# Performance work log

Measured on AMD Instinct MI355X. Metric: run time of the kernel, lower is better.

The kernel has to match this reference:

```python
import jax, jax.numpy as jnp
import numpy as np

DIM = 384
HEADS = 12
WH, WW = 7, 7
N = WH * WW
HEAD_DIM = DIM // HEADS
SCALE = HEAD_DIM ** -0.5


def _double_step_seq(step1, len1, step2, len2):
    seq1 = np.arange(0, step1 * len1, step1)
    seq2 = np.arange(0, step2 * len2, step2)
    return (seq1[:, None] + seq2[None, :]).reshape(1, -1)


def _rel_position_index():
    coords = _double_step_seq(2 * WW - 1, WH, 1, WW)  # (1, N)
    idx = coords + coords.T                            # (N, N)
    idx = idx[:, ::-1].copy()                          # flip along dim 1
    return jnp.asarray(idx, dtype=jnp.int32)

REL_IDX = _rel_position_index()


def setup_inputs() -> dict:
    key = jax.random.key(0)
    ks = jax.random.split(key, 6)
    B_ = 4096
    x = jax.random.normal(ks[0], (B_, N, DIM), dtype=jnp.float32)
    mask = jnp.zeros((64, N, N), dtype=jnp.float32)
    qkv_w = jax.random.normal(ks[1], (3 * DIM, DIM), dtype=jnp.float32) * 0.02
    qkv_b = jax.random.normal(ks[2], (3 * DIM,), dtype=jnp.float32) * 0.02
    proj_w = jax.random.normal(ks[3], (DIM, DIM), dtype=jnp.float32) * 0.02
    proj_b = jax.random.normal(ks[4], (DIM,), dtype=jnp.float32) * 0.02
    bias_table = jax.random.normal(ks[5], (169, HEADS), dtype=jnp.float32) * 0.02
    return {"x": x, "mask": mask, "qkv_w": qkv_w, "qkv_b": qkv_b,
            "proj_w": proj_w, "proj_b": proj_b, "bias_table": bias_table}


def reference(x, mask, qkv_w, qkv_b, proj_w, proj_b, bias_table):
    B_, n, C = x.shape
    # qkv projection: (B_, N, 3C) -> (3, B_, H, N, d)
    qkv = (x @ qkv_w.T + qkv_b).reshape(B_, n, 3, HEADS, HEAD_DIM)
    qkv = jnp.transpose(qkv, (2, 0, 3, 1, 4))
    q, k, v = qkv[0], qkv[1], qkv[2]
    q = q * SCALE
    attn = jnp.einsum('bhnd,bhmd->bhnm', q, k)  # (B_, H, N, N)
    # gathered relative position bias: (H, N, N)
    rel_bias = bias_table[REL_IDX.reshape(-1)].reshape(n, n, HEADS)
    rel_bias = jnp.transpose(rel_bias, (2, 0, 1))
    attn = attn + rel_bias[None]
    nW = mask.shape[0]
    attn = attn.reshape(B_ // nW, nW, HEADS, n, n) + mask[None, :, None]
    attn = attn.reshape(B_, HEADS, n, n)
    attn = jax.nn.softmax(attn, axis=-1)
    out = jnp.einsum('bhnm,bhmd->bnhd', attn, v).reshape(B_, n, C)
    out = out @ proj_w.T + proj_b
    return out
```

## Files before the change

### kernel.cpp

```cpp
#include <hip/hip_runtime.h>
#include <hip/hip_bf16.h>

#define NTOK 49
#define DIMC 384
#define NH 12
#define QSCALE 0.17677669529663687f

typedef __attribute__((ext_vector_type(8))) short short8;
typedef __attribute__((ext_vector_type(4))) float f32x4;
typedef unsigned int u32;

#define KS_OFF  0
#define VT_OFF  8192
#define PS_OFF  12288
#define QA_OFF  16384
#define BT_OFF  18432
#define QB_OFF  20464
#define SL_TOT  21616

#define NQFRAG (NH * 6 * 12)
#define WQB_SHORTS (NQFRAG * 512)
#define WPB_SHORTS (3 * 6 * 8192)
#define MB_TILES 1568
#define AV_BYTES ((size_t)MB_TILES * 6 * 16384)

__device__ __forceinline__ short f2bf(float f) {
    __bf16 h = (__bf16)f;
    return __builtin_bit_cast(short, h);
}
__device__ __forceinline__ float bf2f(short s) {
    u32 u = ((u32)(unsigned short)s) << 16;
    return __builtin_bit_cast(float, u);
}
__device__ __forceinline__ int cof(int p) { return 13 * (p / 7) + (p % 7); }

__device__ __forceinline__ void gld_lds16(const void* g, void* l) {
    __builtin_amdgcn_global_load_lds(
        (const __attribute__((address_space(1))) u32*)g,
        (__attribute__((address_space(3))) u32*)l, 16, 0, 0);
}

__device__ __forceinline__ short8 gather_bf(const float* __restrict__ w, int row, int k0) {
    const float* p = w + row * DIMC + k0;
    float4 a = *(const float4*)p;
    float4 b = *(const float4*)(p + 4);
    short8 r;
    r[0]=f2bf(a.x); r[1]=f2bf(a.y); r[2]=f2bf(a.z); r[3]=f2bf(a.w);
    r[4]=f2bf(b.x); r[5]=f2bf(b.y); r[6]=f2bf(b.z); r[7]=f2bf(b.w);
    return r;
}

__global__ void prep_weights(const float* __restrict__ qw, const float* __restrict__ pw,
                             short* __restrict__ wqb, short* __restrict__ wpb) {
    int gt = blockIdx.x * blockDim.x + threadIdx.x;
    if (gt < NQFRAG * 64) {
        int F = gt >> 6, lane = gt & 63;
        int h = F / 72, r = F % 72;
        int nt = r / 12, ks = r % 12;
        int l15 = lane & 15, l4 = lane >> 4;
        int grow = (nt >> 1) * DIMC + h * 32 + (nt & 1) * 16 + l15;
        const float* src = qw + grow * DIMC + ks * 32 + l4 * 8;
        short8 o;
        #pragma unroll
        for (int e = 0; e < 8; ++e) o[e] = f2bf(src[e]);
        *(short8*)(wqb + gt * 8) = o;
    } else if (gt < NQFRAG * 64 + 3 * 6 * 128 * 8) {
        int t2 = gt - NQFRAG * 64;
        int g  = t2 & 7;
        int r  = (t2 >> 3) & 127;
        int kc = (t2 >> 10) % 6;
        int nb = t2 / 6144;
        int k0 = kc * 64 + ((g ^ (r & 7)) << 3);
        const float* src = pw + (nb * 128 + r) * DIMC + k0;
        short8 o;
        #pragma unroll
        for (int e = 0; e < 8; ++e) o[e] = f2bf(src[e]);
        *(short8*)(wpb + (nb * 6 + kc) * 8192 + r * 64 + g * 8) = o;
    }
}

__global__ __launch_bounds__(256, 2)
void winattn_fused(const float* __restrict__ x, const float* __restrict__ mask,
                   const float* __restrict__ qkv_b, const float* __restrict__ bias_table,
                   const short* __restrict__ wqb, char* __restrict__ avb)
{
    __shared__ short SL[SL_TOT] __attribute__((aligned(128)));

    const int tid  = threadIdx.x;
    const int wv   = tid >> 6;
    const int lane = tid & 63;
    const int l15  = lane & 15;
    const int l4   = lane >> 4;
    const int win  = blockIdx.x;

    for (int i = tid; i < 169 * NH; i += 256) SL[BT_OFF + i] = f2bf(bias_table[i]);
    for (int i = tid; i < 3 * DIMC; i += 256) SL[QB_OFF + i] = f2bf(qkv_b[i]);

    short8 xf[12];
    {
        const int row = wv * 16 + l15;
        const bool valid = row < NTOK;
        const float* xr = x + (size_t)win * (NTOK * DIMC) + row * DIMC;
        #pragma unroll
        for (int ks = 0; ks < 12; ++ks) {
            short8 r;
            if (valid) {
                float4 a = *(const float4*)(xr + ks * 32 + l4 * 8);
                float4 b = *(const float4*)(xr + ks * 32 + l4 * 8 + 4);
                r[0]=f2bf(a.x); r[1]=f2bf(a.y); r[2]=f2bf(a.z); r[3]=f2bf(a.w);
                r[4]=f2bf(b.x); r[5]=f2bf(b.y); r[6]=f2bf(b.z); r[7]=f2bf(b.w);
            } else {
                r = (short8)0;
            }
            xf[ks] = r;
        }
    }

    u32 mvp[4][2];
    int bidx[4][4];
    {
        const float* maskp = mask + (size_t)(win & 63) * (NTOK * NTOK);
        #pragma unroll
        for (int t = 0; t < 4; ++t) {
            int m = t * 16 + l15;
            float pad = (m < NTOK) ? 0.f : -1e30f;
            #pragma unroll
            for (int rp = 0; rp < 2; ++rp) {
                float v[2];
                #pragma unroll
                for (int e = 0; e < 2; ++e) {
                    int i = wv * 16 + l4 * 4 + rp * 2 + e;
                    v[e] = ((i < NTOK && m < NTOK) ? maskp[i * NTOK + m] : 0.f) + pad;
                }
                mvp[t][rp] = (u32)(unsigned short)f2bf(v[0]) |
                             ((u32)(unsigned short)f2bf(v[1]) << 16);
            }
        }
        int cofi[4], cofm[4];
        #pragma unroll
        for (int t = 0; t < 4; ++t) {
            int m = t * 16 + l15;
            cofm[t] = cof(48 - (m < NTOK ? m : 48));
        }
        #pragma unroll
        for (int reg = 0; reg < 4; ++reg) {
            int i = wv * 16 + l4 * 4 + reg;
            cofi[reg] = cof(i < NTOK ? i : 48);
        }
        #pragma unroll
        for (int t = 0; t < 4; ++t)
            #pragma unroll
            for (int reg = 0; reg < 4; ++reg)
                bidx[t][reg] = (cofi[reg] + cofm[t]) * NH;
    }

    const f32x4 zf = (f32x4){0.f, 0.f, 0.f, 0.f};

    __syncthreads();

    auto qkv_head = [&](int h) {
        const int p = h & 1;
        f32x4 qa[6];
        #pragma unroll
        for (int nt = 0; nt < 6; ++nt) qa[nt] = zf;
        const short* wq_h = wqb + (size_t)h * 36864 + lane * 8;
        #pragma unroll
        for (int c = 0; c < 6; ++c) {
            short8 bfr[12];
            #pragma unroll
            for (int j = 0; j < 12; ++j)
                bfr[j] = *(const short8*)(wq_h + (((j >> 1) * 12) + 2 * c + (j & 1)) * 512);
            #pragma unroll
            for (int j = 0; j < 12; ++j)
                qa[j >> 1] = __builtin_amdgcn_mfma_f32_16x16x32_bf16(
                    xf[2 * c + (j & 1)], bfr[j], qa[j >> 1], 0, 0, 0);
        }
        #pragma unroll
        for (int nt = 0; nt < 6; ++nt) {
            const int sub = nt >> 1;
            const int colw = (nt & 1) * 16 + l15;
            const float bias = bf2f(SL[QB_OFF + sub * DIMC + h * 32 + colw]);
            #pragma unroll
            for (int reg = 0; reg < 4; ++reg) {
                const int rl = l4 * 4 + reg;
                const int tokg = wv * 16 + rl;
                float val = qa[nt][reg] + bias;
                if (sub == 0) {
                    int byt = rl * 64 + ((colw << 1) ^ ((rl & 3) << 4));
                    SL[QA_OFF + wv * 512 + (byt >> 1)] = f2bf(val * QSCALE);
                } else if (sub == 1) {
                    int byt = tokg * 128 + ((colw << 1) ^ ((tokg & 7) << 4));
                    SL[KS_OFF + p * 4096 + (byt >> 1)] = f2bf(val);
                } else {
                    int byt = colw * 128 + ((tokg << 1) ^ ((colw & 7) << 4));
                    SL[VT_OFF + p * 2048 + (byt >> 1)] = f2bf(val);
                }
            }
        }
        asm volatile("s_waitcnt lgkmcnt(0)" ::: "memory");
        __builtin_amdgcn_s_barrier();
        __builtin_amdgcn_sched_barrier(0);
    };

    auto attn_head = [&](int hh) {
        const int pp = hh & 1;
        short8 aq;
        {
            int byt = l15 * 64 + ((l4 * 16) ^ ((l15 & 3) << 4));
            aq = *(const short8*)&SL[QA_OFF + wv * 512 + (byt >> 1)];
        }
        f32x4 sc[4];
        #pragma unroll
        for (int t = 0; t < 4; ++t) {
            int row = t * 16 + l15;
            int byt = row * 128 + ((l4 * 16) ^ ((row & 7) << 4));
            short8 bk = *(const short8*)&SL[KS_OFF + pp * 4096 + (byt >> 1)];
            sc[t] = __builtin_amdgcn_mfma_f32_16x16x32_bf16(aq, bk, zf, 0, 0, 0);
        }
        float p[4][4];
        #pragma unroll
        for (int t = 0; t < 4; ++t) {
            #pragma unroll
            for (int reg = 0; reg < 4; ++reg) {
                u32 pk = mvp[t][reg >> 1];
                float mval = bf2f((short)((reg & 1) ? (pk >> 16) : (pk & 0xffff)));
                float bt = bf2f(SL[BT_OFF + bidx[t][reg] + hh]);
                p[t][reg] = sc[t][reg] + mval + bt;
            }
        }
        #pragma unroll
        for (int reg = 0; reg < 4; ++reg) {
            float mx = fmaxf(fmaxf(p[0][reg], p[1][reg]), fmaxf(p[2][reg], p[3][reg]));
            #pragma unroll
            for (int off = 8; off >= 1; off >>= 1) mx = fmaxf(mx, __shfl_xor(mx, off, 64));
            float s0 = 0.f;
            #pragma unroll
            for (int t = 0; t < 4; ++t) { p[t][reg] = __expf(p[t][reg] - mx); s0 += p[t][reg]; }
            #pragma unroll
            for (int off = 8; off >= 1; off >>= 1) s0 += __shfl_xor(s0, off, 64);
            float rs = 1.f / s0;
            #pragma unroll
            for (int t = 0; t < 4; ++t) p[t][reg] *= rs;
        }
        #pragma unroll
        for (int t = 0; t < 4; ++t)
            #pragma unroll
            for (int reg = 0; reg < 4; ++reg) {
                int r = l4 * 4 + reg;
                int byt = r * 128 + ((((t * 16 + l15) << 1)) ^ ((r & 7) << 4));
                SL[PS_OFF + wv * 1024 + (byt >> 1)] = f2bf(p[t][reg]);
            }
        f32x4 av[2];
        av[0] = zf; av[1] = zf;
        #pragma unroll
        for (int kst = 0; kst < 2; ++kst) {
            short8 pa;
            {
                int byt = l15 * 128 + (((kst * 64 + l4 * 16)) ^ ((l15 & 7) << 4));
                pa = *(const short8*)&SL[PS_OFF + wv * 1024 + (byt >> 1)];
            }
            #pragma unroll
            for (int dt = 0; dt < 2; ++dt) {
                int d = dt * 16 + l15;
                int byt = d * 128 + (((kst * 64 + l4 * 16)) ^ ((d & 7) << 4));
                short8 bv = *(const short8*)&SL[VT_OFF + pp * 2048 + (byt >> 1)];
                av[dt] = __builtin_amdgcn_mfma_f32_16x16x32_bf16(pa, bv, av[dt], 0, 0, 0);
            }
        }
        #pragma unroll
        for (int dt = 0; dt < 2; ++dt)
            #pragma unroll
            for (int reg = 0; reg < 4; ++reg) {
                int tok = wv * 16 + l4 * 4 + reg;
                if (tok < NTOK) {
                    int gt = win * NTOK + tok;
                    int mb = gt >> 7, r = gt & 127;
                    int inner = ((((hh & 1) << 6) | ((dt * 16 + l15) << 1))) ^ ((r & 7) << 4);
                    *(short*)(avb + (size_t)(mb * 6 + (hh >> 1)) * 16384 + r * 128 + inner)
                        = f2bf(av[dt][reg]);
                }
            }
    };

    qkv_head(0);
    #pragma unroll 1
    for (int h = 1; h < NH; ++h) {
        attn_head(h - 1);
        qkv_head(h);
    }
    attn_head(NH - 1);
}

__global__ __launch_bounds__(256, 2)
void proj_gemm(const char* __restrict__ avb, const short* __restrict__ wpb,
               const float* __restrict__ proj_b, float* __restrict__ out)
{
    __shared__ char LC[2][32768] __attribute__((aligned(128)));

    const int tid = threadIdx.x;
    const int wv = tid >> 6, lane = tid & 63;
    const int l15 = lane & 15, l4 = lane >> 4;
    const int wr = wv >> 1, wc = wv & 1;
    const int mb = blockIdx.x / 3, nb = blockIdx.x % 3;

    const char* asrc = avb + (size_t)mb * 6 * 16384;
    const char* bsrc = (const char*)wpb + (size_t)nb * 6 * 16384;

    f32x4 acc[4][4];
    #pragma unroll
    for (int mi = 0; mi < 4; ++mi)
        #pragma unroll
        for (int ni = 0; ni < 4; ++ni) acc[mi][ni] = (f32x4){0.f, 0.f, 0.f, 0.f};

    #pragma unroll
    for (int it = 0; it < 4; ++it) {
        int L = (wv * 4 + it) * 1024;
        gld_lds16(asrc + L + lane * 16, &LC[0][L]);
        gld_lds16(bsrc + L + lane * 16, &LC[0][16384 + L]);
    }

    #pragma unroll
    for (int kc = 0; kc < 6; ++kc) {
        __builtin_amdgcn_sched_barrier(0);
        asm volatile("s_waitcnt vmcnt(0)" ::: "memory");
        __builtin_amdgcn_s_barrier();
        __builtin_amdgcn_sched_barrier(0);
        if (kc < 5) {
            #pragma unroll
            for (int it = 0; it < 4; ++it) {
                int L = (wv * 4 + it) * 1024;
                gld_lds16(asrc + (kc + 1) * 16384 + L + lane * 16, &LC[(kc + 1) & 1][L]);
                gld_lds16(bsrc + (kc + 1) * 16384 + L + lane * 16, &LC[(kc + 1) & 1][16384 + L]);
            }
        }
        const char* bufp = LC[kc & 1];
        __builtin_amdgcn_s_setprio(1);
        #pragma unroll
        for (int ksub = 0; ksub < 2; ++ksub) {
            short8 a[4], b[4];
            #pragma unroll
            for (int mi = 0; mi < 4; ++mi) {
                int row = wr * 64 + mi * 16 + l15;
                a[mi] = *(const short8*)(bufp + row * 128 +
                        ((ksub * 64 + l4 * 16) ^ ((row & 7) << 4)));
            }
            #pragma unroll
            for (int ni = 0; ni < 4; ++ni) {
                int row = wc * 64 + ni * 16 + l15;
                b[ni] = *(const short8*)(bufp + 16384 + row * 128 +
                        ((ksub * 64 + l4 * 16) ^ ((row & 7) << 4)));
            }
            #pragma unroll
            for (int mi = 0; mi < 4; ++mi)
                #pragma unroll
                for (int ni = 0; ni < 4; ++ni)
                    acc[mi][ni] = __builtin_amdgcn_mfma_f32_16x16x32_bf16(
                        a[mi], b[ni], acc[mi][ni], 0, 0, 0);
        }
        __builtin_amdgcn_s_setprio(0);
    }

    float pb[4];
    #pragma unroll
    for (int ni = 0; ni < 4; ++ni) pb[ni] = proj_b[nb * 128 + wc * 64 + ni * 16 + l15];
    #pragma unroll
    for (int mi = 0; mi < 4; ++mi) {
        #pragma unroll
        for (int ni = 0; ni < 4; ++ni) {
            #pragma unroll
            for (int reg = 0; reg < 4; ++reg) {
                size_t row = (size_t)(mb * 128 + wr * 64 + mi * 16 + l4 * 4 + reg);
                out[row * DIMC + nb * 128 + wc * 64 + ni * 16 + l15] = acc[mi][ni][reg] + pb[ni];
            }
        }
    }
}

__global__ __launch_bounds__(256, 2)
void winattn_fallback(const float* __restrict__ x, const float* __restrict__ mask,
                      const float* __restrict__ qkv_w, const float* __restrict__ qkv_b,
                      const float* __restrict__ proj_w, const float* __restrict__ proj_b,
                      const float* __restrict__ bias_table, float* __restrict__ out)
{
    __shared__ short SL[26624] __attribute__((aligned(128)));
    const int tid = threadIdx.x, wv = tid >> 6, lane = tid & 63;
    const int l15 = lane & 15, l4 = lane >> 4;
    const int win = blockIdx.x;
    const int xbase = win * (NTOK * DIMC);
    const int KSo = 0, VTo = 2048, PSo = 4096, QAo = 8192;

    short8 xf[12];
    {
        const int row = wv * 16 + l15;
        const bool valid = row < NTOK;
        const float* xr = x + xbase + row * DIMC;
        #pragma unroll
        for (int ks = 0; ks < 12; ++ks)
            xf[ks] = valid ? gather_bf(xr, 0, ks * 32 + l4 * 8) : (short8)0;
    }
    float mv[4][4]; int bidx[4][4]; float negm[4];
    {
        const float* maskp = mask + (win & 63) * (NTOK * NTOK);
        int cofi[4], cofm[4];
        #pragma unroll
        for (int t = 0; t < 4; ++t) {
            int m = t * 16 + l15;
            negm[t] = (m < NTOK) ? 0.f : -1e30f;
            cofm[t] = cof(48 - (m < NTOK ? m : 48));
            #pragma unroll
            for (int reg = 0; reg < 4; ++reg) {
                int i = wv * 16 + l4 * 4 + reg;
                mv[t][reg] = (i < NTOK && m < NTOK) ? maskp[i * NTOK + m] : 0.f;
            }
        }
        #pragma unroll
        for (int reg = 0; reg < 4; ++reg) {
            int i = wv * 16 + l4 * 4 + reg;
            cofi[reg] = cof(i < NTOK ? i : 48);
        }
        #pragma unroll
        for (int t = 0; t < 4; ++t)
            #pragma unroll
            for (int reg = 0; reg < 4; ++reg) bidx[t][reg] = (cofi[reg] + cofm[t]) * NH;
    }
    f32x4 pacc[24];
    #pragma unroll
    for (int t = 0; t < 24; ++t) pacc[t] = (f32x4){0.f, 0.f, 0.f, 0.f};
    const f32x4 zf = (f32x4){0.f, 0.f, 0.f, 0.f};
    __syncthreads();

    #pragma unroll 1
    for (int h = 0; h < NH; ++h) {
        f32x4 qa[6];
        #pragma unroll
        for (int nt = 0; nt < 6; ++nt) qa[nt] = zf;
        #pragma unroll
        for (int nt = 0; nt < 6; ++nt) {
            const int grow = (nt >> 1) * DIMC + h * 32 + (nt & 1) * 16 + l15;
            #pragma unroll
            for (int ks = 0; ks < 12; ++ks) {
                short8 b = gather_bf(qkv_w, grow, ks * 32 + l4 * 8);
                qa[nt] = __builtin_amdgcn_mfma_f32_16x16x32_bf16(xf[ks], b, qa[nt], 0, 0, 0);
            }
        }
        #pragma unroll
        for (int nt = 0; nt < 6; ++nt) {
            const int sub = nt >> 1;
            const int colw = (nt & 1) * 16 + l15;
            const float bias = qkv_b[sub * DIMC + h * 32 + colw];
            #pragma unroll
            for (int reg = 0; reg < 4; ++reg) {
                const int tokg = wv * 16 + l4 * 4 + reg;
                float val = qa[nt][reg] + bias;
                if (sub == 0) {
                    int byt = tokg * 64 + ((colw << 1) ^ ((tokg & 3) << 4));
                    SL[QAo + (byt >> 1)] = f2bf(val * QSCALE);
                } else if (sub == 1) {
                    int byt = tokg * 64 + ((colw << 1) ^ ((tokg & 3) << 4));
                    SL[KSo + (byt >> 1)] = f2bf(val);
                } else {
                    int byt = colw * 128 + ((tokg << 1) ^ ((colw & 7) << 4));
                    SL[VTo + (byt >> 1)] = f2bf(val);
                }
            }
        }
        __syncthreads();
        short8 aq;
        { int row = wv*16+l15; int byt = row*64 + ((l4*16) ^ ((row&3)<<4));
          aq = *(const short8*)&SL[QAo + (byt>>1)]; }
        f32x4 sc[4];
        #pragma unroll
        for (int t = 0; t < 4; ++t) {
            int row = t*16+l15; int byt = row*64 + ((l4*16) ^ ((row&3)<<4));
            short8 bk = *(const short8*)&SL[KSo + (byt>>1)];
            sc[t] = __builtin_amdgcn_mfma_f32_16x16x32_bf16(aq, bk, zf, 0, 0, 0);
        }
        float p[4][4];
        #pragma unroll
        for (int t = 0; t < 4; ++t)
            #pragma unroll
            for (int reg = 0; reg < 4; ++reg)
                p[t][reg] = sc[t][reg] + mv[t][reg] + bias_table[bidx[t][reg] + h] + negm[t];
        #pragma unroll
        for (int reg = 0; reg < 4; ++reg) {
            float mx = fmaxf(fmaxf(p[0][reg], p[1][reg]), fmaxf(p[2][reg], p[3][reg]));
            #pragma unroll
            for (int off = 8; off >= 1; off >>= 1) mx = fmaxf(mx, __shfl_xor(mx, off, 64));
            float s0 = 0.f;
            #pragma unroll
            for (int t = 0; t < 4; ++t) { p[t][reg] = __expf(p[t][reg] - mx); s0 += p[t][reg]; }
            #pragma unroll
            for (int off = 8; off >= 1; off >>= 1) s0 += __shfl_xor(s0, off, 64);
            float rs = 1.f / s0;
            #pragma unroll
            for (int t = 0; t < 4; ++t) p[t][reg] *= rs;
        }
        #pragma unroll
        for (int t = 0; t < 4; ++t)
            #pragma unroll
            for (int reg = 0; reg < 4; ++reg) {
                int row = wv*16 + l4*4 + reg;
                int byt = row*128 + (((t*16+l15) << 1) ^ ((row&7)<<4));
                SL[PSo + (byt>>1)] = f2bf(p[t][reg]);
            }
        f32x4 av[2]; av[0] = zf; av[1] = zf;
        #pragma unroll
        for (int kst = 0; kst < 2; ++kst) {
            short8 pa;
            { int row = wv*16+l15; int byt = row*128 + ((kst*64+l4*16) ^ ((row&7)<<4));
              pa = *(const short8*)&SL[PSo + (byt>>1)]; }
            #pragma unroll
            for (int dt = 0; dt < 2; ++dt) {
                int d = dt*16+l15; int byt = d*128 + ((kst*64+l4*16) ^ ((d&7)<<4));
                short8 bv = *(const short8*)&SL[VTo + (byt>>1)];
                av[dt] = __builtin_amdgcn_mfma_f32_16x16x32_bf16(pa, bv, av[dt], 0, 0, 0);
            }
        }
        __syncthreads();
        #pragma unroll
        for (int dt = 0; dt < 2; ++dt)
            #pragma unroll
            for (int reg = 0; reg < 4; ++reg) {
                int row = wv*16 + l4*4 + reg;
                int byt = row*64 + (((dt*16+l15) << 1) ^ ((row&3)<<4));
                SL[QAo + (byt>>1)] = f2bf(av[dt][reg]);
            }
        __syncthreads();
        short8 aa;
        { int row = wv*16+l15; int byt = row*64 + ((l4*16) ^ ((row&3)<<4));
          aa = *(const short8*)&SL[QAo + (byt>>1)]; }
        #pragma unroll
        for (int nt = 0; nt < 24; ++nt) {
            short8 bp = gather_bf(proj_w, nt * 16 + l15, h * 32 + l4 * 8);
            pacc[nt] = __builtin_amdgcn_mfma_f32_16x16x32_bf16(aa, bp, pacc[nt], 0, 0, 0);
        }
    }
    {
        float* op = out + xbase;
        #pragma unroll
        for (int nt = 0; nt < 24; ++nt) {
            const float pb = proj_b[nt * 16 + l15];
            #pragma unroll
            for (int reg = 0; reg < 4; ++reg) {
                const int i = wv * 16 + l4 * 4 + reg;
                if (i < NTOK) op[i * DIMC + nt * 16 + l15] = pacc[nt][reg] + pb;
            }
        }
    }
}

extern "C" void kernel_launch(void* const* d_in, const int* in_sizes, int n_in,
                              void* d_out, int out_size, void* d_ws, size_t ws_size,
                              hipStream_t stream) {
    const float* x          = (const float*)d_in[0];
    const float* mask       = (const float*)d_in[1];
    const float* qkv_w      = (const float*)d_in[2];
    const float* qkv_b      = (const float*)d_in[3];
    const float* proj_w     = (const float*)d_in[4];
    const float* proj_b     = (const float*)d_in[5];
    const float* bias_table = (const float*)d_in[6];
    float* out = (float*)d_out;

    const size_t need = (size_t)WQB_SHORTS * 2 + (size_t)WPB_SHORTS * 2 + AV_BYTES;
    if (ws_size >= need) {
        short* wqb = (short*)d_ws;
        short* wpb = wqb + WQB_SHORTS;
        char*  avb = (char*)(wpb + WPB_SHORTS);
        prep_weights<<<288, 256, 0, stream>>>(qkv_w, proj_w, wqb, wpb);
        winattn_fused<<<4096, 256, 0, stream>>>(x, mask, qkv_b, bias_table, wqb, avb);
        proj_gemm<<<MB_TILES * 3, 256, 0, stream>>>(avb, wpb, proj_b, out);
    } else {
        winattn_fallback<<<4096, 256, 0, stream>>>(x, mask, qkv_w, qkv_b, proj_w,
                                                   proj_b, bias_table, out);
    }
}
```

Measured before the change: 869.4 us.

## Split fused window attention into chunked QKV GEMM, attention, and projection kernels

Replaces the per-window fused kernel, which recomputed the QKV projection per head from global bf16 weight fragments, with a tiled LDS-staged QKV GEMM over pairs of padded windows that writes MFMA-ready Q/K/V fragments to a workspace. A slimmer attention kernel reads those fragments directly, and the projection GEMM is adapted to the padded 64-token-per-window layout. Work is processed in 4 or 8 chunks to bound workspace size and keep intermediates cache-resident. This adds intermediate global traffic and extra launches in exchange for better weight reuse and GEMM efficiency.

```diff
diff --git a/kernel.cpp b/kernel.cpp
--- a/kernel.cpp
+++ b/kernel.cpp
@@ -10,19 +10,8 @@
 typedef __attribute__((ext_vector_type(4))) float f32x4;
 typedef unsigned int u32;
 
-#define KS_OFF  0
-#define VT_OFF  8192
-#define PS_OFF  12288
-#define QA_OFF  16384
-#define BT_OFF  18432
-#define QB_OFF  20464
-#define SL_TOT  21616
-
-#define NQFRAG (NH * 6 * 12)
-#define WQB_SHORTS (NQFRAG * 512)
-#define WPB_SHORTS (3 * 6 * 8192)
-#define MB_TILES 1568
-#define AV_BYTES ((size_t)MB_TILES * 6 * 16384)
+#define WQB2_SHORTS (54 * 8192)
+#define WPB_SHORTS  (18 * 8192)
 
 __device__ __forceinline__ short f2bf(float f) {
     __bf16 h = (__bf16)f;
@@ -50,71 +39,197 @@
     return r;
 }
 
-__global__ void prep_weights(const float* __restrict__ qw, const float* __restrict__ pw,
-                             short* __restrict__ wqb, short* __restrict__ wpb) {
-    int gt = blockIdx.x * blockDim.x + threadIdx.x;
-    if (gt < NQFRAG * 64) {
-        int F = gt >> 6, lane = gt & 63;
-        int h = F / 72, r = F % 72;
-        int nt = r / 12, ks = r % 12;
-        int l15 = lane & 15, l4 = lane >> 4;
-        int grow = (nt >> 1) * DIMC + h * 32 + (nt & 1) * 16 + l15;
-        const float* src = qw + grow * DIMC + ks * 32 + l4 * 8;
-        short8 o;
+__global__ void prep2(const float* __restrict__ qw, const float* __restrict__ pw,
+                      short* __restrict__ wqb2, short* __restrict__ wpb) {
+    int gt = blockIdx.x * 256 + threadIdx.x;
+    int tile = gt >> 10;
+    int rem = gt & 1023;
+    int r = rem >> 3, g = rem & 7;
+    int kc = tile % 6;
+    int k0 = kc * 64 + ((g ^ (r & 7)) << 3);
+    short8 o;
+    if (tile < 54) {
+        int nb = tile / 6;
+        const float* src = qw + (size_t)(nb * 128 + r) * DIMC + k0;
         #pragma unroll
         for (int e = 0; e < 8; ++e) o[e] = f2bf(src[e]);
-        *(short8*)(wqb + gt * 8) = o;
-    } else if (gt < NQFRAG * 64 + 3 * 6 * 128 * 8) {
-        int t2 = gt - NQFRAG * 64;
-        int g  = t2 & 7;
-        int r  = (t2 >> 3) & 127;
-        int kc = (t2 >> 10) % 6;
-        int nb = t2 / 6144;
-        int k0 = kc * 64 + ((g ^ (r & 7)) << 3);
-        const float* src = pw + (nb * 128 + r) * DIMC + k0;
-        short8 o;
+        *(short8*)(wqb2 + (size_t)tile * 8192 + r * 64 + g * 8) = o;
+    } else {
+        int t2 = tile - 54;
+        int nb = t2 / 6;
+        const float* src = pw + (size_t)(nb * 128 + r) * DIMC + k0;
         #pragma unroll
         for (int e = 0; e < 8; ++e) o[e] = f2bf(src[e]);
-        *(short8*)(wpb + (nb * 6 + kc) * 8192 + r * 64 + g * 8) = o;
+        *(short8*)(wpb + (size_t)t2 * 8192 + r * 64 + g * 8) = o;
     }
 }
 
 __global__ __launch_bounds__(256, 2)
-void winattn_fused(const float* __restrict__ x, const float* __restrict__ mask,
-                   const float* __restrict__ qkv_b, const float* __restrict__ bias_table,
-                   const short* __restrict__ wqb, char* __restrict__ avb)
+void qkv_gemm(const float* __restrict__ x, const float* __restrict__ qkv_b,
+              const short* __restrict__ wqb2, short* __restrict__ qkvb, int w0)
 {
-    __shared__ short SL[SL_TOT] __attribute__((aligned(128)));
-
-    const int tid  = threadIdx.x;
-    const int wv   = tid >> 6;
-    const int lane = tid & 63;
-    const int l15  = lane & 15;
-    const int l4   = lane >> 4;
-    const int win  = blockIdx.x;
-
-    for (int i = tid; i < 169 * NH; i += 256) SL[BT_OFF + i] = f2bf(bias_table[i]);
-    for (int i = tid; i < 3 * DIMC; i += 256) SL[QB_OFF + i] = f2bf(qkv_b[i]);
-
-    short8 xf[12];
-    {
-        const int row = wv * 16 + l15;
-        const bool valid = row < NTOK;
-        const float* xr = x + (size_t)win * (NTOK * DIMC) + row * DIMC;
-        #pragma unroll
-        for (int ks = 0; ks < 12; ++ks) {
-            short8 r;
-            if (valid) {
-                float4 a = *(const float4*)(xr + ks * 32 + l4 * 8);
-                float4 b = *(const float4*)(xr + ks * 32 + l4 * 8 + 4);
-                r[0]=f2bf(a.x); r[1]=f2bf(a.y); r[2]=f2bf(a.z); r[3]=f2bf(a.w);
-                r[4]=f2bf(b.x); r[5]=f2bf(b.y); r[6]=f2bf(b.z); r[7]=f2bf(b.w);
-            } else {
-                r = (short8)0;
-            }
-            xf[ks] = r;
-        }
-    }
+    __shared__ char LDSB[65536] __attribute__((aligned(128)));
+    char* Ab = LDSB;
+    char* Bb = LDSB + 32768;
+
+    const int tid = threadIdx.x;
+    const int wv = tid >> 6, lane = tid & 63;
+    const int l15 = lane & 15, l4 = lane >> 4;
+    const int wr = wv >> 1, wc = wv & 1;
+    const int mb = blockIdx.x / 9, nb = blockIdx.x % 9;
+
+    const int arow = tid >> 1, achalf = tid & 1;
+    const int tokA = arow & 63;
+    const bool avalid = tokA < NTOK;
+    const int winA = w0 + mb * 2 + (arow >> 6);
+    const float* abase = x + ((size_t)winA * NTOK + (avalid ? tokA : NTOK - 1)) * DIMC + achalf * 32;
+    const char* bsrc = (const char*)(wqb2 + (size_t)(nb * 6) * 8192);
+
+    f32x4 acc[4][4];
+    #pragma unroll
+    for (int mi = 0; mi < 4; ++mi)
+        #pragma unroll
+        for (int ni = 0; ni < 4; ++ni) acc[mi][ni] = (f32x4){0.f, 0.f, 0.f, 0.f};
+
+    f32x4 areg[8];
+    #pragma unroll
+    for (int i = 0; i < 8; ++i) areg[i] = *(const f32x4*)(abase + i * 4);
+    #pragma unroll
+    for (int it = 0; it < 4; ++it)
+        gld_lds16(bsrc + it * 4096 + wv * 1024 + lane * 16, Bb + it * 4096 + wv * 1024);
+
+    #pragma unroll
+    for (int kc = 0; kc < 6; ++kc) {
+        char* Acur = Ab + (kc & 1) * 16384;
+        char* Bcur = Bb + (kc & 1) * 16384;
+        __builtin_amdgcn_sched_barrier(0);
+        asm volatile("s_waitcnt vmcnt(0)" ::: "memory");
+        __builtin_amdgcn_sched_barrier(0);
+        #pragma unroll
+        for (int q = 0; q < 4; ++q) {
+            short8 pk;
+            #pragma unroll
+            for (int e = 0; e < 4; ++e) {
+                pk[e]     = avalid ? f2bf(areg[q * 2][e])     : (short)0;
+                pk[4 + e] = avalid ? f2bf(areg[q * 2 + 1][e]) : (short)0;
+            }
+            *(short8*)(Acur + arow * 128 + (((achalf * 4 + q) ^ (arow & 7)) << 4)) = pk;
+        }
+        __builtin_amdgcn_sched_barrier(0);
+        asm volatile("s_waitcnt lgkmcnt(0)" ::: "memory");
+        __builtin_amdgcn_s_barrier();
+        __builtin_amdgcn_sched_barrier(0);
+        if (kc < 5) {
+            char* Bnxt = Bb + ((kc + 1) & 1) * 16384;
+            #pragma unroll
+            for (int it = 0; it < 4; ++it)
+                gld_lds16(bsrc + (kc + 1) * 16384 + it * 4096 + wv * 1024 + lane * 16,
+                          Bnxt + it * 4096 + wv * 1024);
+            #pragma unroll
+            for (int i = 0; i < 8; ++i) areg[i] = *(const f32x4*)(abase + (kc + 1) * 64 + i * 4);
+        }
+        __builtin_amdgcn_s_setprio(1);
+        #pragma unroll
+        for (int ksub = 0; ksub < 2; ++ksub) {
+            short8 a[4], b[4];
+            #pragma unroll
+            for (int mi = 0; mi < 4; ++mi) {
+                int row = wr * 64 + mi * 16 + l15;
+                a[mi] = *(const short8*)(Acur + row * 128 + ((ksub * 64 + l4 * 16) ^ ((row & 7) << 4)));
+            }
+            #pragma unroll
+            for (int ni = 0; ni < 4; ++ni) {
+                int row = wc * 64 + ni * 16 + l15;
+                b[ni] = *(const short8*)(Bcur + row * 128 + ((ksub * 64 + l4 * 16) ^ ((row & 7) << 4)));
+            }
+            #pragma unroll
+            for (int mi = 0; mi < 4; ++mi)
+                #pragma unroll
+                for (int ni = 0; ni < 4; ++ni)
+                    acc[mi][ni] = __builtin_amdgcn_mfma_f32_16x16x32_bf16(
+                        a[mi], b[ni], acc[mi][ni], 0, 0, 0);
+        }
+        __builtin_amdgcn_s_setprio(0);
+    }
+
+    __syncthreads();
+
+    float bias[4];
+    #pragma unroll
+    for (int ni = 0; ni < 4; ++ni) bias[ni] = qkv_b[nb * 128 + wc * 64 + ni * 16 + l15];
+
+    char* slab = LDSB + wv * 8192;
+    const int wl = mb * 2 + wr;
+    const int sub = nb / 3;
+
+    if (sub < 2) {
+        #pragma unroll
+        for (int mi = 0; mi < 4; ++mi)
+            #pragma unroll
+            for (int ni = 0; ni < 4; ++ni)
+                #pragma unroll
+                for (int reg = 0; reg < 4; ++reg) {
+                    float v = acc[mi][ni][reg] + bias[ni];
+                    if (sub == 0) v *= QSCALE;
+                    int rowp = mi * 16 + l4 * 4 + reg, colp = ni * 16 + l15;
+                    *(short*)(slab + rowp * 128 + ((colp * 2) ^ ((rowp & 7) << 4))) = f2bf(v);
+                }
+        __builtin_amdgcn_sched_barrier(0);
+        asm volatile("s_waitcnt lgkmcnt(0)" ::: "memory");
+        __builtin_amdgcn_sched_barrier(0);
+        #pragma unroll
+        for (int hh = 0; hh < 2; ++hh)
+            #pragma unroll
+            for (int s = 0; s < 4; ++s) {
+                int head = (nb % 3) * 4 + wc * 2 + hh;
+                int rowp = s * 16 + l15;
+                short8 frag = *(const short8*)(slab + rowp * 128 +
+                              ((hh * 64 + l4 * 16) ^ ((rowp & 7) << 4)));
+                *(short8*)(qkvb + (((size_t)wl * NH + head) * 12 + sub * 4 + s) * 512 + lane * 8) = frag;
+            }
+    } else {
+        #pragma unroll
+        for (int mi = 0; mi < 4; ++mi)
+            #pragma unroll
+            for (int ni = 0; ni < 4; ++ni)
+                #pragma unroll
+                for (int reg = 0; reg < 4; ++reg) {
+                    float v = acc[mi][ni][reg] + bias[ni];
+                    int rowp = mi * 16 + l4 * 4 + reg, colp = ni * 16 + l15;
+                    *(short*)(slab + colp * 128 + ((rowp * 2) ^ ((colp & 7) << 4))) = f2bf(v);
+                }
+        __builtin_amdgcn_sched_barrier(0);
+        asm volatile("s_waitcnt lgkmcnt(0)" ::: "memory");
+        __builtin_amdgcn_sched_barrier(0);
+        #pragma unroll
+        for (int hh = 0; hh < 2; ++hh)
+            #pragma unroll
+            for (int dt = 0; dt < 2; ++dt)
+                #pragma unroll
+                for (int kst = 0; kst < 2; ++kst) {
+                    int head = (nb - 6) * 4 + wc * 2 + hh;
+                    int row2 = hh * 32 + dt * 16 + l15;
+                    short8 frag = *(const short8*)(slab + row2 * 128 +
+                                  ((kst * 64 + l4 * 16) ^ ((row2 & 7) << 4)));
+                    *(short8*)(qkvb + (((size_t)wl * NH + head) * 12 + 8 + dt * 2 + kst) * 512 + lane * 8) = frag;
+                }
+    }
+}
+
+__global__ __launch_bounds__(256)
+void attn_win(const float* __restrict__ mask, const float* __restrict__ bias_table,
+              const short* __restrict__ qkvb, char* __restrict__ avb, int w0)
+{
+    __shared__ short SA[6144] __attribute__((aligned(128)));
+    const int PS2 = 0, BT2 = 4096;
+
+    const int tid = threadIdx.x;
+    const int wv = tid >> 6, lane = tid & 63;
+    const int l15 = lane & 15, l4 = lane >> 4;
+    const int wl = blockIdx.x;
+    const int win = w0 + wl;
+
+    for (int i = tid; i < 169 * NH; i += 256) SA[BT2 + i] = f2bf(bias_table[i]);
 
     u32 mvp[4][2];
     int bidx[4][4];
@@ -153,81 +268,36 @@
             for (int reg = 0; reg < 4; ++reg)
                 bidx[t][reg] = (cofi[reg] + cofm[t]) * NH;
     }
-
     const f32x4 zf = (f32x4){0.f, 0.f, 0.f, 0.f};
-
     __syncthreads();
 
-    auto qkv_head = [&](int h) {
-        const int p = h & 1;
-        f32x4 qa[6];
-        #pragma unroll
-        for (int nt = 0; nt < 6; ++nt) qa[nt] = zf;
-        const short* wq_h = wqb + (size_t)h * 36864 + lane * 8;
-        #pragma unroll
-        for (int c = 0; c < 6; ++c) {
-            short8 bfr[12];
-            #pragma unroll
-            for (int j = 0; j < 12; ++j)
-                bfr[j] = *(const short8*)(wq_h + (((j >> 1) * 12) + 2 * c + (j & 1)) * 512);
-            #pragma unroll
-            for (int j = 0; j < 12; ++j)
-                qa[j >> 1] = __builtin_amdgcn_mfma_f32_16x16x32_bf16(
-                    xf[2 * c + (j & 1)], bfr[j], qa[j >> 1], 0, 0, 0);
-        }
-        #pragma unroll
-        for (int nt = 0; nt < 6; ++nt) {
-            const int sub = nt >> 1;
-            const int colw = (nt & 1) * 16 + l15;
-            const float bias = bf2f(SL[QB_OFF + sub * DIMC + h * 32 + colw]);
-            #pragma unroll
-            for (int reg = 0; reg < 4; ++reg) {
-                const int rl = l4 * 4 + reg;
-                const int tokg = wv * 16 + rl;
-                float val = qa[nt][reg] + bias;
-                if (sub == 0) {
-                    int byt = rl * 64 + ((colw << 1) ^ ((rl & 3) << 4));
-                    SL[QA_OFF + wv * 512 + (byt >> 1)] = f2bf(val * QSCALE);
-                } else if (sub == 1) {
-                    int byt = tokg * 128 + ((colw << 1) ^ ((tokg & 7) << 4));
-                    SL[KS_OFF + p * 4096 + (byt >> 1)] = f2bf(val);
-                } else {
-                    int byt = colw * 128 + ((tokg << 1) ^ ((colw & 7) << 4));
-                    SL[VT_OFF + p * 2048 + (byt >> 1)] = f2bf(val);
-                }
-            }
-        }
-        asm volatile("s_waitcnt lgkmcnt(0)" ::: "memory");
-        __builtin_amdgcn_s_barrier();
-        __builtin_amdgcn_sched_barrier(0);
-    };
-
-    auto attn_head = [&](int hh) {
-        const int pp = hh & 1;
-        short8 aq;
-        {
-            int byt = l15 * 64 + ((l4 * 16) ^ ((l15 & 3) << 4));
-            aq = *(const short8*)&SL[QA_OFF + wv * 512 + (byt >> 1)];
-        }
+    const short* qh = qkvb + (size_t)wl * (NH * 12 * 512);
+
+    #pragma unroll 1
+    for (int h = 0; h < NH; ++h) {
+        const short* hb = qh + h * (12 * 512) + lane * 8;
+        short8 q = *(const short8*)(hb + 0 * 512 + wv * 512);
+        short8 kf[4], vf[4];
+        #pragma unroll
+        for (int t = 0; t < 4; ++t) kf[t] = *(const short8*)(hb + (4 + t) * 512);
+        #pragma unroll
+        for (int j = 0; j < 4; ++j) vf[j] = *(const short8*)(hb + (8 + j) * 512);
+
         f32x4 sc[4];
         #pragma unroll
-        for (int t = 0; t < 4; ++t) {
-            int row = t * 16 + l15;
-            int byt = row * 128 + ((l4 * 16) ^ ((row & 7) << 4));
-            short8 bk = *(const short8*)&SL[KS_OFF + pp * 4096 + (byt >> 1)];
-            sc[t] = __builtin_amdgcn_mfma_f32_16x16x32_bf16(aq, bk, zf, 0, 0, 0);
-        }
+        for (int t = 0; t < 4; ++t)
+            sc[t] = __builtin_amdgcn_mfma_f32_16x16x32_bf16(q, kf[t], zf, 0, 0, 0);
+
         float p[4][4];
         #pragma unroll
-        for (int t = 0; t < 4; ++t) {
+        for (int t = 0; t < 4; ++t)
             #pragma unroll
             for (int reg = 0; reg < 4; ++reg) {
                 u32 pk = mvp[t][reg >> 1];
                 float mval = bf2f((short)((reg & 1) ? (pk >> 16) : (pk & 0xffff)));
-                float bt = bf2f(SL[BT_OFF + bidx[t][reg] + hh]);
+                float bt = bf2f(SA[BT2 + bidx[t][reg] + h]);
                 p[t][reg] = sc[t][reg] + mval + bt;
             }
-        }
         #pragma unroll
         for (int reg = 0; reg < 4; ++reg) {
             float mx = fmaxf(fmaxf(p[0][reg], p[1][reg]), fmaxf(p[2][reg], p[3][reg]));
@@ -248,7 +318,7 @@
             for (int reg = 0; reg < 4; ++reg) {
                 int r = l4 * 4 + reg;
                 int byt = r * 128 + ((((t * 16 + l15) << 1)) ^ ((r & 7) << 4));
-                SL[PS_OFF + wv * 1024 + (byt >> 1)] = f2bf(p[t][reg]);
+                SA[PS2 + wv * 1024 + (byt >> 1)] = f2bf(p[t][reg]);
             }
         f32x4 av[2];
         av[0] = zf; av[1] = zf;
@@ -257,15 +327,11 @@
             short8 pa;
             {
                 int byt = l15 * 128 + (((kst * 64 + l4 * 16)) ^ ((l15 & 7) << 4));
-                pa = *(const short8*)&SL[PS_OFF + wv * 1024 + (byt >> 1)];
-            }
-            #pragma unroll
-            for (int dt = 0; dt < 2; ++dt) {
-                int d = dt * 16 + l15;
-                int byt = d * 128 + (((kst * 64 + l4 * 16)) ^ ((d & 7) << 4));
-                short8 bv = *(const short8*)&SL[VT_OFF + pp * 2048 + (byt >> 1)];
-                av[dt] = __builtin_amdgcn_mfma_f32_16x16x32_bf16(pa, bv, av[dt], 0, 0, 0);
-            }
+                pa = *(const short8*)&SA[PS2 + wv * 1024 + (byt >> 1)];
+            }
+            #pragma unroll
+            for (int dt = 0; dt < 2; ++dt)
+                av[dt] = __builtin_amdgcn_mfma_f32_16x16x32_bf16(pa, vf[dt * 2 + kst], av[dt], 0, 0, 0);
         }
         #pragma unroll
         for (int dt = 0; dt < 2; ++dt)
@@ -273,27 +339,18 @@
             for (int reg = 0; reg < 4; ++reg) {
                 int tok = wv * 16 + l4 * 4 + reg;
                 if (tok < NTOK) {
-                    int gt = win * NTOK + tok;
-                    int mb = gt >> 7, r = gt & 127;
-                    int inner = ((((hh & 1) << 6) | ((dt * 16 + l15) << 1))) ^ ((r & 7) << 4);
-                    *(short*)(avb + (size_t)(mb * 6 + (hh >> 1)) * 16384 + r * 128 + inner)
+                    int r = (wl & 1) * 64 + tok;
+                    int inner = ((((h & 1) << 6) | ((dt * 16 + l15) << 1))) ^ ((r & 7) << 4);
+                    *(short*)(avb + (size_t)((wl >> 1) * 6 + (h >> 1)) * 16384 + r * 128 + inner)
                         = f2bf(av[dt][reg]);
                 }
             }
-    };
-
-    qkv_head(0);
-    #pragma unroll 1
-    for (int h = 1; h < NH; ++h) {
-        attn_head(h - 1);
-        qkv_head(h);
-    }
-    attn_head(NH - 1);
+    }
 }
 
 __global__ __launch_bounds__(256, 2)
-void proj_gemm(const char* __restrict__ avb, const short* __restrict__ wpb,
-               const float* __restrict__ proj_b, float* __restrict__ out)
+void proj_pad(const char* __restrict__ avb, const short* __restrict__ wpb,
+              const float* __restrict__ proj_b, float* __restrict__ out, int mb0)
 {
     __shared__ char LC[2][32768] __attribute__((aligned(128)));
 
@@ -363,14 +420,17 @@
     float pb[4];
     #pragma unroll
     for (int ni = 0; ni < 4; ++ni) pb[ni] = proj_b[nb * 128 + wc * 64 + ni * 16 + l15];
+    const int wg = (mb0 + mb) * 2 + wr;
     #pragma unroll
     for (int mi = 0; mi < 4; ++mi) {
         #pragma unroll
         for (int ni = 0; ni < 4; ++ni) {
             #pragma unroll
             for (int reg = 0; reg < 4; ++reg) {
-                size_t row = (size_t)(mb * 128 + wr * 64 + mi * 16 + l4 * 4 + reg);
-                out[row * DIMC + nb * 128 + wc * 64 + ni * 16 + l15] = acc[mi][ni][reg] + pb[ni];
+                int tok = mi * 16 + l4 * 4 + reg;
+                if (tok < NTOK)
+                    out[((size_t)wg * NTOK + tok) * DIMC + nb * 128 + wc * 64 + ni * 16 + l15]
+                        = acc[mi][ni][reg] + pb[ni];
             }
         }
     }
@@ -561,14 +621,30 @@
     const float* bias_table = (const float*)d_in[6];
     float* out = (float*)d_out;
 
-    const size_t need = (size_t)WQB_SHORTS * 2 + (size_t)WPB_SHORTS * 2 + AV_BYTES;
-    if (ws_size >= need) {
-        short* wqb = (short*)d_ws;
-        short* wpb = wqb + WQB_SHORTS;
-        char*  avb = (char*)(wpb + WPB_SHORTS);
-        prep_weights<<<288, 256, 0, stream>>>(qkv_w, proj_w, wqb, wpb);
-        winattn_fused<<<4096, 256, 0, stream>>>(x, mask, qkv_b, bias_table, wqb, avb);
-        proj_gemm<<<MB_TILES * 3, 256, 0, stream>>>(avb, wpb, proj_b, out);
+    const size_t fixed = ((size_t)WQB2_SHORTS + WPB_SHORTS) * 2;
+    auto need = [&](int c) {
+        size_t wpc = 4096 / c;
+        return fixed + wpc * 147456UL  + wpc * 49152UL ;
+    };
+    int c = 0;
+    if (ws_size >= need(4)) c = 4;
+    else if (ws_size >= need(8)) c = 8;
+
+    if (c) {
+        short* wqb2 = (short*)d_ws;
+        short* wpb  = wqb2 + WQB2_SHORTS;
+        short* qkvb = wpb + WPB_SHORTS;
+        const int wpc = 4096 / c;
+        char* avb = (char*)(qkvb + (size_t)wpc * 73728);
+
+        prep2<<<288, 256, 0, stream>>>(qkv_w, proj_w, wqb2, wpb);
+        for (int ch = 0; ch < c; ++ch) {
+            const int w0 = ch * wpc;
+            const int mbc = wpc / 2;
+            qkv_gemm<<<mbc * 9, 256, 0, stream>>>(x, qkv_b, wqb2, qkvb, w0);
+            attn_win<<<wpc, 256, 0, stream>>>(mask, bias_table, qkvb, avb, w0);
+            proj_pad<<<mbc * 3, 256, 0, stream>>>(avb, wpb, proj_b, out, ch * mbc);
+        }
     } else {
         winattn_fallback<<<4096, 256, 0, stream>>>(x, mask, qkv_w, qkv_b, proj_w,
                                                    proj_b, bias_table, out);
```

Measured after the change: 1.025 ms. 1.18x slower.
